# Optimization experiments

Hardware: AMD Instinct MI355X
Metric: run time of the kernel (lower is better)

## Reference

```python
import jax, jax.numpy as jnp
import numpy as np


def setup_inputs() -> dict:
    key = jax.random.key(0)
    ks = jax.random.split(key, 7)
    B, N, F, H = 128, 64, 128, 128
    s1 = 1.0 / np.sqrt(2 * N)  # torch Linear default-ish scaling
    s2 = 1.0 / np.sqrt(H)
    return {
        "agent_features": jax.random.normal(ks[0], (B, N, F), dtype=jnp.float32),
        "W1": jax.random.normal(ks[1], (2 * N, H), dtype=jnp.float32) * s1,
        "b1": jax.random.normal(ks[2], (H,), dtype=jnp.float32) * s1,
        "W2": jax.random.normal(ks[3], (H, H), dtype=jnp.float32) * s2,
        "b2": jax.random.normal(ks[4], (H,), dtype=jnp.float32) * s2,
        "w3": jax.random.normal(ks[5], (H,), dtype=jnp.float32) * s2,
        "b3": jax.random.normal(ks[6], (1,), dtype=jnp.float32) * s2,
        "mixing_weights": jnp.ones((N,), dtype=jnp.float32) / N,
    }


def reference(agent_features, W1, b1, W2, b2, w3, b3, mixing_weights):
    N = mixing_weights.shape[0]
    f = agent_features[:, :, :N]  # [B, N, N] (first num_agents features)
    # Split first Linear's weight into the i-half and j-half of the concat:
    # concat([f_i, f_j]) @ W1 == f_i @ W1[:N] + f_j @ W1[N:]
    Ai = jnp.einsum('bnf,fh->bnh', f, W1[:N])   # contribution of agent i
    Aj = jnp.einsum('bnf,fh->bnh', f, W1[N:])   # contribution of agent j
    h1 = jax.nn.relu(Ai[:, :, None, :] + Aj[:, None, :, :] + b1)  # [B,N,N,H]
    h2 = jax.nn.relu(jnp.einsum('bijh,hk->bijk', h1, W2) + b2)    # [B,N,N,H]
    correlations = jax.nn.sigmoid(jnp.einsum('bijh,h->bij', h2, w3) + b3[0])
    weights = jax.nn.softmax(mixing_weights, axis=0)
    return correlations, weights
```

## Files before the change

kernel.cpp:

```cpp
#include <hip/hip_runtime.h>
#include <hip/hip_bf16.h>


typedef __bf16 bf16x8 __attribute__((ext_vector_type(8)));
typedef float f32x4 __attribute__((ext_vector_type(4)));

#define B_SZ 128
#define N_SZ 64
#define H_SZ 128

__global__ __launch_bounds__(256) void setup_kernel(
    const float* __restrict__ af, const float* __restrict__ W1,
    const float* __restrict__ b1, const float* __restrict__ W2,
    const float* __restrict__ mw, float* __restrict__ AiP,
    float* __restrict__ Aj, unsigned short* __restrict__ W2T,
    float* __restrict__ outw)
{
  const int blk = blockIdx.x;
  const int tid = threadIdx.x;

  if (blk < 2048) {
    __shared__ float fl[4 * 64];
    const int bn0 = blk << 2;
    fl[tid] = af[((bn0 + (tid >> 6)) << 7) + (tid & 63)];
    __syncthreads();
    const int h    = tid & 127;
    const int half = tid >> 7;
    const float* Wp = W1 + ((half << 6) << 7) + h;
    float acc0 = 0.f, acc1 = 0.f, acc2 = 0.f, acc3 = 0.f;
#pragma unroll
    for (int fq = 0; fq < 16; ++fq) {
      const float w0 = Wp[(fq * 4 + 0) << 7];
      const float w1v = Wp[(fq * 4 + 1) << 7];
      const float w2v = Wp[(fq * 4 + 2) << 7];
      const float w3v = Wp[(fq * 4 + 3) << 7];
      const float4 f0 = *(const float4*)&fl[0 * 64 + (fq << 2)];
      const float4 f1 = *(const float4*)&fl[1 * 64 + (fq << 2)];
      const float4 f2 = *(const float4*)&fl[2 * 64 + (fq << 2)];
      const float4 f3 = *(const float4*)&fl[3 * 64 + (fq << 2)];
      acc0 = fmaf(f0.x, w0, fmaf(f0.y, w1v, fmaf(f0.z, w2v, fmaf(f0.w, w3v, acc0))));
      acc1 = fmaf(f1.x, w0, fmaf(f1.y, w1v, fmaf(f1.z, w2v, fmaf(f1.w, w3v, acc1))));
      acc2 = fmaf(f2.x, w0, fmaf(f2.y, w1v, fmaf(f2.z, w2v, fmaf(f2.w, w3v, acc2))));
      acc3 = fmaf(f3.x, w0, fmaf(f3.y, w1v, fmaf(f3.z, w2v, fmaf(f3.w, w3v, acc3))));
    }
    if (half == 0) {
      const float bb = b1[h];
      AiP[((bn0 + 0) << 7) + h] = acc0 + bb;
      AiP[((bn0 + 1) << 7) + h] = acc1 + bb;
      AiP[((bn0 + 2) << 7) + h] = acc2 + bb;
      AiP[((bn0 + 3) << 7) + h] = acc3 + bb;
    } else {
      Aj[((bn0 + 0) << 7) + h] = acc0;
      Aj[((bn0 + 1) << 7) + h] = acc1;
      Aj[((bn0 + 2) << 7) + h] = acc2;
      Aj[((bn0 + 3) << 7) + h] = acc3;
    }
  } else if (blk < 2112) {
    int idx = ((blk - 2048) << 8) + tid;
    int k = idx >> 7, n = idx & 127;
    unsigned u = __float_as_uint(W2[idx]);
    u += 0x7fffu + ((u >> 16) & 1u);
    W2T[(n << 7) + k] = (unsigned short)(u >> 16);
  } else {
    if (tid < 64) {
      float v = mw[tid];
      float m = v;
      for (int off = 32; off > 0; off >>= 1) m = fmaxf(m, __shfl_xor(m, off));
      float e = expf(v - m);
      float s = e;
      for (int off = 32; off > 0; off >>= 1) s += __shfl_xor(s, off);
      outw[tid] = e / s;
    }
  }
}

__global__ __launch_bounds__(512, 4) void corr_kernel(
    const float* __restrict__ AiP, const float* __restrict__ Aj,
    const unsigned short* __restrict__ W2T,
    const float* __restrict__ b2, const float* __restrict__ w3,
    const float* __restrict__ b3, float* __restrict__ out)
{
  __shared__ __align__(16) unsigned short W2s[128 * 128];
  __shared__ __align__(16) float AjF[64 * 132];
  __shared__ __align__(16) float AiF[16 * 132];
  __shared__ float b2s[128], w3s[128];
  __shared__ float part[2][2][128];

  const int tid  = threadIdx.x;
  const int lane = tid & 63;
  const int wave = tid >> 6;
  const int c = lane & 15, g = lane >> 4;
  const int wm = wave & 1;
  const int wn = wave >> 1;

  const int blk = blockIdx.x;
  const int b   = blk >> 2;
  const int ip0 = (blk & 3) << 3;

  {
    const uint4* src = (const uint4*)W2T;
#pragma unroll
    for (int it = 0; it < 4; ++it) {
      const int idx = (it << 9) + tid;
      const int n = idx >> 4, e = idx & 15;
      const uint4 v = src[idx];
      *(uint4*)&W2s[(n << 7) + ((e ^ (n & 15)) << 3)] = v;
    }
  }
  {
    const float4* src = (const float4*)(Aj + (b << 13));
#pragma unroll
    for (int p = 0; p < 4; ++p) {
      const int idx = (p << 9) + tid;
      const int r = idx >> 5, u = idx & 31;
      *(float4*)&AjF[r * 132 + (u << 2)] = src[idx];
    }
    const float4* srcA = (const float4*)(AiP + (((b << 6) + (ip0 << 1)) << 7));
    {
      const int r = tid >> 5, u = tid & 31;
      *(float4*)&AiF[r * 132 + (u << 2)] = srcA[tid];
    }
    if (tid < 128) b2s[tid] = b2[tid];
    else if (tid < 256) w3s[tid - 128] = w3[tid - 128];
  }

  const float bias3 = b3[0];

  const int j0 = ((wn << 5) + c) & 63;
  const int j1 = ((wn << 5) + 16 + c) & 63;
  const float* ajb0 = &AjF[j0 * 132 + (g << 3)];
  const float* ajb1 = &AjF[j1 * 132 + (g << 3)];
  const int i_sel = wn >> 1;

  __syncthreads();

  for (int t = 0; t < 8; ++t) {
    const float* aib = &AiF[((t << 1) + i_sel) * 132 + (g << 3)];

    f32x4 acc[4][2];
#pragma unroll
    for (int mt = 0; mt < 4; ++mt) {
      const f32x4 bv = *(const f32x4*)&b2s[(wm << 6) + (mt << 4) + (g << 2)];
      acc[mt][0] = bv;
      acc[mt][1] = bv;
    }

#pragma unroll
    for (int kt = 0; kt < 4; ++kt) {
      const int es = ((kt << 2) + g) ^ c;
      bf16x8 wv[4];
#pragma unroll
      for (int mt = 0; mt < 4; ++mt)
        wv[mt] = *(const bf16x8*)&W2s[(((wm << 6) + (mt << 4) + c) << 7) + (es << 3)];

      const f32x4 a0 = *(const f32x4*)(aib + (kt << 5));
      const f32x4 a1 = *(const f32x4*)(aib + (kt << 5) + 4);
      bf16x8 hv[2];
#pragma unroll
      for (int tn = 0; tn < 2; ++tn) {
        const float* ajb = tn ? ajb1 : ajb0;
        const f32x4 c0 = *(const f32x4*)(ajb + (kt << 5));
        const f32x4 c1 = *(const f32x4*)(ajb + (kt << 5) + 4);
        const f32x4 h0 = a0 + c0;
        const f32x4 h1v = a1 + c1;
#pragma unroll
        for (int e = 0; e < 4; ++e) {
          hv[tn][e]     = (__bf16)fmaxf(h0[e], 0.f);
          hv[tn][e + 4] = (__bf16)fmaxf(h1v[e], 0.f);
        }
      }

#pragma unroll
      for (int mt = 0; mt < 4; ++mt)
#pragma unroll
        for (int tn = 0; tn < 2; ++tn)
          acc[mt][tn] = __builtin_amdgcn_mfma_f32_16x16x32_bf16(
              wv[mt], hv[tn], acc[mt][tn], 0, 0, 0);
    }

    float s0 = 0.f, s1 = 0.f;
#pragma unroll
    for (int mt = 0; mt < 4; ++mt) {
      const f32x4 wv3 = *(const f32x4*)&w3s[(wm << 6) + (mt << 4) + (g << 2)];
#pragma unroll
      for (int p = 0; p < 4; ++p) {
        s0 = fmaf(fmaxf(acc[mt][0][p], 0.f), wv3[p], s0);
        s1 = fmaf(fmaxf(acc[mt][1][p], 0.f), wv3[p], s1);
      }
    }
    s0 += __shfl_xor(s0, 16);
    s0 += __shfl_xor(s0, 32);
    s1 += __shfl_xor(s1, 16);
    s1 += __shfl_xor(s1, 32);

    const int pb = t & 1;
    if (g == 0) {
      part[pb][wm][(wn << 5) + c]      = s0;
      part[pb][wm][(wn << 5) + 16 + c] = s1;
    }

    __syncthreads();

    if (tid < 128) {
      const float v = part[pb][0][tid] + part[pb][1][tid] + bias3;
      out[(b << 12) + ((ip0 + t) << 7) + tid] = 1.f / (1.f + __expf(-v));
    }
  }
}

extern "C" void kernel_launch(void* const* d_in, const int* in_sizes, int n_in,
                              void* d_out, int out_size, void* d_ws,
                              size_t ws_size, hipStream_t stream)
{
  const float* af = (const float*)d_in[0];
  const float* W1 = (const float*)d_in[1];
  const float* b1 = (const float*)d_in[2];
  const float* W2 = (const float*)d_in[3];
  const float* b2 = (const float*)d_in[4];
  const float* w3 = (const float*)d_in[5];
  const float* b3 = (const float*)d_in[6];
  const float* mw = (const float*)d_in[7];
  float* out = (float*)d_out;

  float* AiP = (float*)d_ws;
  float* Aj  = AiP + B_SZ * N_SZ * H_SZ;
  unsigned short* W2T = (unsigned short*)(Aj + B_SZ * N_SZ * H_SZ);

  setup_kernel<<<2113, 256, 0, stream>>>(af, W1, b1, W2, mw, AiP, Aj, W2T,
                                         out + B_SZ * N_SZ * N_SZ);
  corr_kernel<<<512, 512, 0, stream>>>(AiP, Aj, W2T, b2, w3, b3, out);
}
```

Measured before the change: 102.1 us.

## Keep W2 and Aj fragments in registers and double rows per block

Each block now covers 32 i-rows (16 iterations) instead of 16, which halves the grid and the number of times W2 and Aj are staged into LDS. The W2 MFMA fragments and the Aj operands are loaded once into registers before the loop, so the per-iteration LDS reads go away. The cost is much higher register pressure (launch bounds occupancy hint lowered from 4 to 2) and fewer blocks in flight, only 256 workgroups on the GPU.

```diff
diff --git a/kernel.cpp b/kernel.cpp
--- a/kernel.cpp
+++ b/kernel.cpp
@@ -74,7 +74,7 @@
   }
 }
 
-__global__ __launch_bounds__(512, 4) void corr_kernel(
+__global__ __launch_bounds__(512, 2) void corr_kernel(
     const float* __restrict__ AiP, const float* __restrict__ Aj,
     const unsigned short* __restrict__ W2T,
     const float* __restrict__ b2, const float* __restrict__ w3,
@@ -82,7 +82,7 @@
 {
   __shared__ __align__(16) unsigned short W2s[128 * 128];
   __shared__ __align__(16) float AjF[64 * 132];
-  __shared__ __align__(16) float AiF[16 * 132];
+  __shared__ __align__(16) float AiF[32 * 132];
   __shared__ float b2s[128], w3s[128];
   __shared__ float part[2][2][128];
 
@@ -94,8 +94,9 @@
   const int wn = wave >> 1;
 
   const int blk = blockIdx.x;
-  const int b   = blk >> 2;
-  const int ip0 = (blk & 3) << 3;
+  const int b   = blk >> 1;
+  const int ih  = blk & 1;
+  const int ip0 = ih << 4;
 
   {
     const uint4* src = (const uint4*)W2T;
@@ -115,26 +116,42 @@
       const int r = idx >> 5, u = idx & 31;
       *(float4*)&AjF[r * 132 + (u << 2)] = src[idx];
     }
-    const float4* srcA = (const float4*)(AiP + (((b << 6) + (ip0 << 1)) << 7));
-    {
-      const int r = tid >> 5, u = tid & 31;
-      *(float4*)&AiF[r * 132 + (u << 2)] = srcA[tid];
+    const float4* srcA = (const float4*)(AiP + (((b << 6) + (ih << 5)) << 7));
+#pragma unroll
+    for (int p = 0; p < 2; ++p) {
+      const int idx = (p << 9) + tid;
+      const int r = idx >> 5, u = idx & 31;
+      *(float4*)&AiF[r * 132 + (u << 2)] = srcA[idx];
     }
     if (tid < 128) b2s[tid] = b2[tid];
     else if (tid < 256) w3s[tid - 128] = w3[tid - 128];
   }
 
   const float bias3 = b3[0];
-
-  const int j0 = ((wn << 5) + c) & 63;
-  const int j1 = ((wn << 5) + 16 + c) & 63;
-  const float* ajb0 = &AjF[j0 * 132 + (g << 3)];
-  const float* ajb1 = &AjF[j1 * 132 + (g << 3)];
   const int i_sel = wn >> 1;
 
   __syncthreads();
 
-  for (int t = 0; t < 8; ++t) {
+  bf16x8 w2r[4][4];
+#pragma unroll
+  for (int mt = 0; mt < 4; ++mt)
+#pragma unroll
+    for (int kt = 0; kt < 4; ++kt) {
+      const int es = ((kt << 2) + g) ^ c;
+      w2r[mt][kt] = *(const bf16x8*)&W2s[(((wm << 6) + (mt << 4) + c) << 7) + (es << 3)];
+    }
+  f32x4 ajr[4][2][2];
+#pragma unroll
+  for (int kt = 0; kt < 4; ++kt)
+#pragma unroll
+    for (int tn = 0; tn < 2; ++tn) {
+      const int j = ((wn << 5) + (tn << 4) + c) & 63;
+      const float* ajb = &AjF[j * 132 + (g << 3) + (kt << 5)];
+      ajr[kt][tn][0] = *(const f32x4*)(ajb);
+      ajr[kt][tn][1] = *(const f32x4*)(ajb + 4);
+    }
+
+  for (int t = 0; t < 16; ++t) {
     const float* aib = &AiF[((t << 1) + i_sel) * 132 + (g << 3)];
 
     f32x4 acc[4][2];
@@ -147,35 +164,25 @@
 
 #pragma unroll
     for (int kt = 0; kt < 4; ++kt) {
-      const int es = ((kt << 2) + g) ^ c;
-      bf16x8 wv[4];
-#pragma unroll
-      for (int mt = 0; mt < 4; ++mt)
-        wv[mt] = *(const bf16x8*)&W2s[(((wm << 6) + (mt << 4) + c) << 7) + (es << 3)];
-
       const f32x4 a0 = *(const f32x4*)(aib + (kt << 5));
       const f32x4 a1 = *(const f32x4*)(aib + (kt << 5) + 4);
       bf16x8 hv[2];
 #pragma unroll
       for (int tn = 0; tn < 2; ++tn) {
-        const float* ajb = tn ? ajb1 : ajb0;
-        const f32x4 c0 = *(const f32x4*)(ajb + (kt << 5));
-        const f32x4 c1 = *(const f32x4*)(ajb + (kt << 5) + 4);
-        const f32x4 h0 = a0 + c0;
-        const f32x4 h1v = a1 + c1;
+        const f32x4 h0 = a0 + ajr[kt][tn][0];
+        const f32x4 h1v = a1 + ajr[kt][tn][1];
 #pragma unroll
         for (int e = 0; e < 4; ++e) {
           hv[tn][e]     = (__bf16)fmaxf(h0[e], 0.f);
           hv[tn][e + 4] = (__bf16)fmaxf(h1v[e], 0.f);
         }
       }
-
 #pragma unroll
       for (int mt = 0; mt < 4; ++mt)
 #pragma unroll
         for (int tn = 0; tn < 2; ++tn)
           acc[mt][tn] = __builtin_amdgcn_mfma_f32_16x16x32_bf16(
-              wv[mt], hv[tn], acc[mt][tn], 0, 0, 0);
+              w2r[mt][kt], hv[tn], acc[mt][tn], 0, 0, 0);
     }
 
     float s0 = 0.f, s1 = 0.f;
@@ -228,5 +235,5 @@
 
   setup_kernel<<<2113, 256, 0, stream>>>(af, W1, b1, W2, mw, AiP, Aj, W2T,
                                          out + B_SZ * N_SZ * N_SZ);
-  corr_kernel<<<512, 512, 0, stream>>>(AiP, Aj, W2T, b2, w3, b3, out);
+  corr_kernel<<<256, 512, 0, stream>>>(AiP, Aj, W2T, b2, w3, b3, out);
 }
```

Result: no change. 102.9 us (+0.7%).
